# Optimization experiments

Measured on AMD Instinct MI355X. Metric: run time of the kernel, lower is better.

The kernel has to match this reference:

```python
import jax, jax.numpy as jnp
import numpy as np

HIDDEN_DIM = 1024
NUM_HEADS = 16
HEAD_DIM = HIDDEN_DIM // NUM_HEADS
SCALAR_NORM = float(np.sqrt(HIDDEN_DIM / NUM_HEADS))


def setup_inputs() -> dict:
    key = jax.random.key(0)
    k1, k2 = jax.random.split(key)
    B, N, D = 2, 2048, HIDDEN_DIM
    x = jax.random.normal(k1, (B, N, D), dtype=jnp.float32)
    # torch Linear weight shape: (3D, D); xavier_uniform-like scale
    limit = float(np.sqrt(6.0 / (D + 3 * D)))
    W_qkv = jax.random.uniform(k2, (3 * D, D), dtype=jnp.float32, minval=-limit, maxval=limit)
    return {"x": x, "W_qkv": W_qkv}


def reference(x, W_qkv):
    b, n, d = x.shape
    h, hd = NUM_HEADS, HEAD_DIM
    qkv = x @ W_qkv.T  # (B, N, 3D)
    q, k, v = jnp.split(qkv, 3, axis=-1)
    # (B, H, N, hd)
    q = q.reshape(b, n, h, hd).transpose(0, 2, 1, 3)
    k = k.reshape(b, n, h, hd).transpose(0, 2, 1, 3)
    v = v.reshape(b, n, h, hd).transpose(0, 2, 1, 3)
    scores = jnp.einsum('bhik,bhjk->bhij', q, k) / SCALAR_NORM
    attn = jax.nn.softmax(scores, axis=-1)
    out = jnp.einsum('bhij,bhjk->bhik', attn, v)
    return out.transpose(0, 2, 1, 3).reshape(b, n, d)
```

## Files before the change

### kernel.cpp

```cpp
#include <hip/hip_runtime.h>
#include <hip/hip_bf16.h>

#define SEQ 2048
#define DMODEL 1024
#define NHEADS 16
#define HD 64
#define BATCH 2

typedef short bf16x8 __attribute__((ext_vector_type(8)));
typedef float f32x4 __attribute__((ext_vector_type(4)));

static __device__ inline ushort f2bf(float f) {
    unsigned u = __float_as_uint(f);
    return (ushort)((u + 0x7fffu + ((u >> 16) & 1u)) >> 16);
}

static __device__ inline unsigned pk2bf(float a, float b) {
    __hip_bfloat162 h = __float22bfloat162_rn(make_float2(a, b));
    union { __hip_bfloat162 h; unsigned u; } c; c.h = h;
    return c.u;
}

static __device__ inline void async16(const ushort* g, ushort* l) {
    __builtin_amdgcn_global_load_lds((const __attribute__((address_space(1))) void*)g,
                                     (__attribute__((address_space(3))) void*)l, 16, 0, 0);
}

__global__ void cvt2(const float* __restrict__ a, ushort* __restrict__ da, int na,
                     const float* __restrict__ b, ushort* __restrict__ db, int nb) {
    long i = (long)(blockIdx.x * blockDim.x + threadIdx.x) * 4;
    const float* s; ushort* d;
    if (i < na) { s = a + i; d = da + i; }
    else { long j = i - na; if (j >= nb) return; s = b + j; d = db + j; }
    float4 v = *(const float4*)s;
    ushort4 o; o.x = f2bf(v.x); o.y = f2bf(v.y); o.z = f2bf(v.z); o.w = f2bf(v.w);
    *(ushort4*)d = o;
}

union GemmSmem {
    struct { ushort A[128 * 64]; ushort B[128 * 64]; } st;
    ushort C[128 * 128];
};

__global__ __launch_bounds__(256) void qkv_gemm(
        const ushort* __restrict__ X, const ushort* __restrict__ W,
        ushort* __restrict__ Qd, ushort* __restrict__ Kd, ushort* __restrict__ Vd) {
    __shared__ GemmSmem sm;
    const int t = threadIdx.x;
    const int lane = t & 63, l15 = lane & 15, quad = lane >> 4;
    const int w = t >> 6, wm = w >> 1, wn = w & 1;
    const int gm = blockIdx.x, gn = blockIdx.y;
    const int srow = t >> 3, scol = (t & 7) * 8;

    f32x4 acc[4][4] = {};

    for (int kt = 0; kt < 16; ++kt) {
        const int k0 = kt * 64;
        __syncthreads();
#pragma unroll
        for (int inst = 0; inst < 4; ++inst) {
            async16(&X[(gm * 128 + inst * 32 + srow) * 1024 + k0 + scol], &sm.st.A[inst * 2048 + t * 8]);
            async16(&W[(gn * 128 + inst * 32 + srow) * 1024 + k0 + scol], &sm.st.B[inst * 2048 + t * 8]);
        }
        __syncthreads();
#pragma unroll
        for (int ks = 0; ks < 2; ++ks) {
            const int kk = ks * 32 + quad * 8;
            bf16x8 af[4], bfr[4];
#pragma unroll
            for (int i = 0; i < 4; ++i) {
                af[i]  = *(const bf16x8*)&sm.st.A[(wm * 64 + i * 16 + l15) * 64 + kk];
                bfr[i] = *(const bf16x8*)&sm.st.B[(wn * 64 + i * 16 + l15) * 64 + kk];
            }
#pragma unroll
            for (int i = 0; i < 4; ++i)
#pragma unroll
                for (int j = 0; j < 4; ++j)
                    acc[i][j] = __builtin_amdgcn_mfma_f32_16x16x32_bf16(af[i], bfr[j], acc[i][j], 0, 0, 0);
        }
    }

    __syncthreads();
    const float sc = (gn < 8) ? (0.125f * 1.44269504f) : 1.0f;
#pragma unroll
    for (int i = 0; i < 4; ++i)
#pragma unroll
        for (int reg = 0; reg < 4; ++reg) {
            const int row = wm * 64 + i * 16 + quad * 4 + reg;
            const int sw = (row & 7) * 8;
#pragma unroll
            for (int jp = 0; jp < 4; jp += 2) {
                unsigned u = pk2bf(acc[i][jp][reg] * sc, acc[i][jp + 1][reg] * sc);
                sm.C[row * 128 + ((wn * 64 + jp * 16 + l15) ^ sw)] = (ushort)u;
                sm.C[row * 128 + ((wn * 64 + (jp + 1) * 16 + l15) ^ sw)] = (ushort)(u >> 16);
            }
        }
    __syncthreads();

    const int which = gn >> 3;
    ushort* dst = (which == 0) ? Qd : ((which == 1) ? Kd : Vd);
    const int rloc = t >> 4, l = t & 15;
#pragma unroll
    for (int pass = 0; pass < 8; ++pass) {
        const int r = pass * 16 + rloc;
        bf16x8 v = *(const bf16x8*)&sm.C[r * 128 + ((l * 8) ^ ((r & 7) * 8))];
        const int ng = gm * 128 + r;
        const int b = ng >> 11, n = ng & 2047;
        const int cl = (gn * 128 + l * 8) & 1023;
        const int h = cl >> 6, hd = cl & 63;
        *(bf16x8*)&dst[(((b * NHEADS + h) * SEQ) + n) * HD + hd] = v;
    }
}

__global__ __launch_bounds__(256) void tr_v(const ushort* __restrict__ src, ushort* __restrict__ dst) {
    __shared__ ushort sT[64][72];
    const int t = threadIdx.x;
    const int bh = blockIdx.y, nt = blockIdx.x;
    const int r0 = t >> 3, c8 = (t & 7) * 8;
    const ushort* sp = src + ((long)bh * SEQ + nt * 64) * HD;
#pragma unroll
    for (int rr = 0; rr < 64; rr += 32)
        *(bf16x8*)&sT[rr + r0][c8] = *(const bf16x8*)&sp[(rr + r0) * HD + c8];
    __syncthreads();
    ushort* dp = dst + (long)bh * HD * SEQ + nt * 64;
#pragma unroll
    for (int rr = 0; rr < 64; rr += 32) {
        const int hd = rr + r0;
        bf16x8 v;
#pragma unroll
        for (int j = 0; j < 8; ++j) v[j] = (short)sT[c8 + j][hd];
        *(bf16x8*)&dp[(long)hd * SEQ + c8] = v;
    }
}

__global__ __launch_bounds__(128, 2) void attn_kernel(
        const ushort* __restrict__ Q, const ushort* __restrict__ K,
        const ushort* __restrict__ VT, float* __restrict__ O) {
    __shared__ ushort sK[64][72];
    __shared__ ushort sVT[64][72];
    __shared__ ushort sP[64][72];
    const int t = threadIdx.x;
    const int lane = t & 63, l15 = lane & 15, quad = lane >> 4;
    const int w = t >> 6;
    const int qt = blockIdx.x, bh = blockIdx.y;
    const ushort* Qp = Q + ((long)bh * SEQ + qt * 64) * HD;
    const ushort* Kp = K + (long)bh * SEQ * HD;
    const ushort* Vp = VT + (long)bh * HD * SEQ;
    const int r0 = t >> 3, c8 = (t & 7) * 8;

    bf16x8 aq[2][2];
#pragma unroll
    for (int st = 0; st < 2; ++st)
#pragma unroll
        for (int kc = 0; kc < 2; ++kc)
            aq[st][kc] = *(const bf16x8*)&Qp[(w * 32 + st * 16 + l15) * HD + kc * 32 + quad * 8];

    f32x4 accO[2][4] = {};
    f32x4 accL[2] = {};
    bf16x8 ones;
#pragma unroll
    for (int j = 0; j < 8; ++j) ones[j] = (short)0x3F80;

    for (int kt = 0; kt < 32; ++kt) {
        __syncthreads();
#pragma unroll
        for (int rr = 0; rr < 64; rr += 16) {
            *(bf16x8*)&sK[rr + r0][c8]  = *(const bf16x8*)&Kp[(kt * 64 + rr + r0) * HD + c8];
            *(bf16x8*)&sVT[rr + r0][c8] = *(const bf16x8*)&Vp[(rr + r0) * SEQ + kt * 64 + c8];
        }
        __syncthreads();

        f32x4 s[2][4];
#pragma unroll
        for (int st = 0; st < 2; ++st)
#pragma unroll
            for (int nb = 0; nb < 4; ++nb) {
                f32x4 z = {};
                z = __builtin_amdgcn_mfma_f32_16x16x32_bf16(aq[st][0], *(const bf16x8*)&sK[nb * 16 + l15][quad * 8], z, 0, 0, 0);
                z = __builtin_amdgcn_mfma_f32_16x16x32_bf16(aq[st][1], *(const bf16x8*)&sK[nb * 16 + l15][32 + quad * 8], z, 0, 0, 0);
                s[st][nb] = z;
            }

#pragma unroll
        for (int st = 0; st < 2; ++st)
#pragma unroll
            for (int r = 0; r < 4; ++r) {
                const int row = w * 32 + st * 16 + quad * 4 + r;
#pragma unroll
                for (int nb = 0; nb < 4; nb += 2) {
                    unsigned u = pk2bf(exp2f(s[st][nb][r]), exp2f(s[st][nb + 1][r]));
                    sP[row][(nb * 16 + l15) ^ (quad << 4)] = (ushort)u;
                    sP[row][((nb + 1) * 16 + l15) ^ (quad << 4)] = (ushort)(u >> 16);
                }
            }

        bf16x8 ap[2][2];
#pragma unroll
        for (int st = 0; st < 2; ++st)
#pragma unroll
            for (int kb = 0; kb < 2; ++kb)
                ap[st][kb] = *(const bf16x8*)&sP[w * 32 + st * 16 + l15][(kb * 32 + quad * 8) ^ ((l15 & 12) << 2)];

#pragma unroll
        for (int st = 0; st < 2; ++st) {
#pragma unroll
            for (int ob = 0; ob < 4; ++ob)
#pragma unroll
                for (int kb = 0; kb < 2; ++kb)
                    accO[st][ob] = __builtin_amdgcn_mfma_f32_16x16x32_bf16(
                        ap[st][kb], *(const bf16x8*)&sVT[ob * 16 + l15][kb * 32 + quad * 8], accO[st][ob], 0, 0, 0);
#pragma unroll
            for (int kb = 0; kb < 2; ++kb)
                accL[st] = __builtin_amdgcn_mfma_f32_16x16x32_bf16(ap[st][kb], ones, accL[st], 0, 0, 0);
        }
    }

    const int b = bh >> 4, h = bh & 15;
#pragma unroll
    for (int st = 0; st < 2; ++st)
#pragma unroll
        for (int r = 0; r < 4; ++r) {
            const float inv = 1.0f / accL[st][r];
            const int row = qt * 64 + w * 32 + st * 16 + quad * 4 + r;
#pragma unroll
            for (int ob = 0; ob < 4; ++ob)
                O[((long)b * SEQ + row) * DMODEL + h * HD + ob * 16 + l15] = accO[st][ob][r] * inv;
        }
}

extern "C" void kernel_launch(void* const* d_in, const int* in_sizes, int n_in,
                              void* d_out, int out_size, void* d_ws, size_t ws_size,
                              hipStream_t stream) {
    const float* x  = (const float*)d_in[0];
    const float* Wq = (const float*)d_in[1];
    float* out = (float*)d_out;

    const int NX = BATCH * SEQ * DMODEL;
    const int NW = 3 * DMODEL * DMODEL;
    const int NQKV = BATCH * NHEADS * SEQ * HD;

    ushort* xb = (ushort*)d_ws;
    ushort* wb = xb + NX;
    ushort* q  = wb + NW;
    ushort* k  = q + NQKV;
    ushort* vtmp = k + NQKV;
    ushort* vt = xb;

    cvt2<<<(NX + NW) / 4 / 256, 256, 0, stream>>>(x, xb, NX, Wq, wb, NW);

    dim3 g1(4096 / 128, 3072 / 128);
    qkv_gemm<<<g1, 256, 0, stream>>>(xb, wb, q, k, vtmp);

    dim3 gt(SEQ / 64, BATCH * NHEADS);
    tr_v<<<gt, 256, 0, stream>>>(vtmp, vt);

    dim3 g2(SEQ / 64, BATCH * NHEADS);
    attn_kernel<<<g2, 128, 0, stream>>>(q, k, vt, out);
}
```

Before: 194.6 us.

## Restructure attention kernel with 32x32 MFMA, register softmax, double-buffered async K/V

The attention kernel now runs 8 waves per block over 256 query rows and uses 32x32x16 MFMA with S computed transposed, so P stays in registers and is repacked via v_permlane32_swap instead of going through shared memory. K and V^T tiles are double-buffered with global_load_lds async copies into XOR-swizzled LDS, and the row sum is kept as a register accumulator instead of an extra MFMA against ones. A remapped block index groups heads for locality, and setprio hints favour MFMA issue. The goal is more K/V reuse per block, fewer LDS round trips and barriers, and overlap of loads with compute, at the cost of higher register pressure and reliance on the permlane/swizzle layout being correct.

```diff
diff --git a/kernel.cpp b/kernel.cpp
--- a/kernel.cpp
+++ b/kernel.cpp
@@ -9,6 +9,7 @@
 
 typedef short bf16x8 __attribute__((ext_vector_type(8)));
 typedef float f32x4 __attribute__((ext_vector_type(4)));
+typedef float f32x16 __attribute__((ext_vector_type(16)));
 
 static __device__ inline ushort f2bf(float f) {
     unsigned u = __float_as_uint(f);
@@ -24,6 +25,10 @@
 static __device__ inline void async16(const ushort* g, ushort* l) {
     __builtin_amdgcn_global_load_lds((const __attribute__((address_space(1))) void*)g,
                                      (__attribute__((address_space(3))) void*)l, 16, 0, 0);
+}
+
+static __device__ inline void plane32swap(unsigned& a, unsigned& b) {
+    asm volatile("v_permlane32_swap_b32 %0, %1" : "+v"(a), "+v"(b));
 }
 
 __global__ void cvt2(const float* __restrict__ a, ushort* __restrict__ da, int na,
@@ -133,99 +138,119 @@
     }
 }
 
-__global__ __launch_bounds__(128, 2) void attn_kernel(
+__global__ __launch_bounds__(512, 2) void attn_kernel(
         const ushort* __restrict__ Q, const ushort* __restrict__ K,
         const ushort* __restrict__ VT, float* __restrict__ O) {
-    __shared__ ushort sK[64][72];
-    __shared__ ushort sVT[64][72];
-    __shared__ ushort sP[64][72];
+    __shared__ ushort sK[2][64 * 64];
+    __shared__ ushort sVT[2][64 * 64];
+    __shared__ float sL[8][32];
+
     const int t = threadIdx.x;
-    const int lane = t & 63, l15 = lane & 15, quad = lane >> 4;
+    const int lane = t & 63, l31 = lane & 31, hi = lane >> 5;
     const int w = t >> 6;
-    const int qt = blockIdx.x, bh = blockIdx.y;
-    const ushort* Qp = Q + ((long)bh * SEQ + qt * 64) * HD;
+
+    const int flat = blockIdx.y * gridDim.x + blockIdx.x;
+    const int qt = (flat >> 3) & 7;
+    const int bh = (flat & 7) + ((flat >> 6) << 3);
+
+    const ushort* Qp = Q + ((long)bh * SEQ + qt * 256 + w * 32) * HD;
     const ushort* Kp = K + (long)bh * SEQ * HD;
     const ushort* Vp = VT + (long)bh * HD * SEQ;
-    const int r0 = t >> 3, c8 = (t & 7) * 8;
-
-    bf16x8 aq[2][2];
-#pragma unroll
-    for (int st = 0; st < 2; ++st)
-#pragma unroll
-        for (int kc = 0; kc < 2; ++kc)
-            aq[st][kc] = *(const bf16x8*)&Qp[(w * 32 + st * 16 + l15) * HD + kc * 32 + quad * 8];
-
-    f32x4 accO[2][4] = {};
-    f32x4 accL[2] = {};
-    bf16x8 ones;
-#pragma unroll
-    for (int j = 0; j < 8; ++j) ones[j] = (short)0x3F80;
+
+    bf16x8 bq[4];
+#pragma unroll
+    for (int ks = 0; ks < 4; ++ks)
+        bq[ks] = *(const bf16x8*)&Qp[l31 * HD + ks * 16 + hi * 8];
+
+    const int sr = t >> 3;
+    const int scc = ((t & 7) ^ (sr & 7)) * 8;
+    const ushort* gK = Kp + sr * HD + scc;
+    const ushort* gV = Vp + (long)sr * SEQ + scc;
+    ushort* lK[2] = { &sK[0][t * 8], &sK[1][t * 8] };
+    ushort* lV[2] = { &sVT[0][t * 8], &sVT[1][t * 8] };
+
+    f32x16 accO[2] = {};
+    float Lp = 0.f;
+    const int swz = (l31 & 7) << 3;
+
+    async16(gK, lK[0]);
+    async16(gV, lV[0]);
+    __syncthreads();
 
     for (int kt = 0; kt < 32; ++kt) {
+        const int cur = kt & 1;
+        if (kt < 31) {
+            async16(gK + (kt + 1) * 64 * HD, lK[cur ^ 1]);
+            async16(gV + (kt + 1) * 64,      lV[cur ^ 1]);
+        }
+        const ushort* bK = sK[cur];
+        const ushort* bV = sVT[cur];
+
+        f32x16 s[2];
+#pragma unroll
+        for (int nb = 0; nb < 2; ++nb) {
+            f32x16 z = {};
+            __builtin_amdgcn_s_setprio(1);
+#pragma unroll
+            for (int ks = 0; ks < 4; ++ks) {
+                bf16x8 ak = *(const bf16x8*)&bK[(nb * 32 + l31) * 64 + ((ks * 16 + hi * 8) ^ swz)];
+                z = __builtin_amdgcn_mfma_f32_32x32x16_bf16(ak, bq[ks], z, 0, 0, 0);
+            }
+            __builtin_amdgcn_s_setprio(0);
+            s[nb] = z;
+        }
+
+        bf16x8 pa[4];
+#pragma unroll
+        for (int nb = 0; nb < 2; ++nb) {
+            float p[16];
+#pragma unroll
+            for (int r = 0; r < 16; ++r) { p[r] = exp2f(s[nb][r]); Lp += p[r]; }
+#pragma unroll
+            for (int h2 = 0; h2 < 2; ++h2) {
+                const int b = 8 * h2;
+                unsigned c0 = pk2bf(p[b + 0], p[b + 1]);
+                unsigned c1 = pk2bf(p[b + 2], p[b + 3]);
+                unsigned c2 = pk2bf(p[b + 4], p[b + 5]);
+                unsigned c3 = pk2bf(p[b + 6], p[b + 7]);
+                plane32swap(c0, c2);
+                plane32swap(c1, c3);
+                union { unsigned u[4]; bf16x8 v; } f;
+                f.u[0] = c0; f.u[1] = c1; f.u[2] = c2; f.u[3] = c3;
+                pa[nb * 2 + h2] = f.v;
+            }
+        }
+
+        __builtin_amdgcn_s_setprio(1);
+#pragma unroll
+        for (int db = 0; db < 2; ++db)
+#pragma unroll
+            for (int ks = 0; ks < 4; ++ks) {
+                bf16x8 vf = *(const bf16x8*)&bV[(db * 32 + l31) * 64 + ((ks * 16 + hi * 8) ^ swz)];
+                accO[db] = __builtin_amdgcn_mfma_f32_32x32x16_bf16(pa[ks], vf, accO[db], 0, 0, 0);
+            }
+        __builtin_amdgcn_s_setprio(0);
+
         __syncthreads();
-#pragma unroll
-        for (int rr = 0; rr < 64; rr += 16) {
-            *(bf16x8*)&sK[rr + r0][c8]  = *(const bf16x8*)&Kp[(kt * 64 + rr + r0) * HD + c8];
-            *(bf16x8*)&sVT[rr + r0][c8] = *(const bf16x8*)&Vp[(rr + r0) * SEQ + kt * 64 + c8];
-        }
-        __syncthreads();
-
-        f32x4 s[2][4];
-#pragma unroll
-        for (int st = 0; st < 2; ++st)
-#pragma unroll
-            for (int nb = 0; nb < 4; ++nb) {
-                f32x4 z = {};
-                z = __builtin_amdgcn_mfma_f32_16x16x32_bf16(aq[st][0], *(const bf16x8*)&sK[nb * 16 + l15][quad * 8], z, 0, 0, 0);
-                z = __builtin_amdgcn_mfma_f32_16x16x32_bf16(aq[st][1], *(const bf16x8*)&sK[nb * 16 + l15][32 + quad * 8], z, 0, 0, 0);
-                s[st][nb] = z;
-            }
-
-#pragma unroll
-        for (int st = 0; st < 2; ++st)
-#pragma unroll
-            for (int r = 0; r < 4; ++r) {
-                const int row = w * 32 + st * 16 + quad * 4 + r;
-#pragma unroll
-                for (int nb = 0; nb < 4; nb += 2) {
-                    unsigned u = pk2bf(exp2f(s[st][nb][r]), exp2f(s[st][nb + 1][r]));
-                    sP[row][(nb * 16 + l15) ^ (quad << 4)] = (ushort)u;
-                    sP[row][((nb + 1) * 16 + l15) ^ (quad << 4)] = (ushort)(u >> 16);
-                }
-            }
-
-        bf16x8 ap[2][2];
-#pragma unroll
-        for (int st = 0; st < 2; ++st)
-#pragma unroll
-            for (int kb = 0; kb < 2; ++kb)
-                ap[st][kb] = *(const bf16x8*)&sP[w * 32 + st * 16 + l15][(kb * 32 + quad * 8) ^ ((l15 & 12) << 2)];
-
-#pragma unroll
-        for (int st = 0; st < 2; ++st) {
-#pragma unroll
-            for (int ob = 0; ob < 4; ++ob)
-#pragma unroll
-                for (int kb = 0; kb < 2; ++kb)
-                    accO[st][ob] = __builtin_amdgcn_mfma_f32_16x16x32_bf16(
-                        ap[st][kb], *(const bf16x8*)&sVT[ob * 16 + l15][kb * 32 + quad * 8], accO[st][ob], 0, 0, 0);
-#pragma unroll
-            for (int kb = 0; kb < 2; ++kb)
-                accL[st] = __builtin_amdgcn_mfma_f32_16x16x32_bf16(ap[st][kb], ones, accL[st], 0, 0, 0);
-        }
-    }
+    }
+
+    unsigned lu = __float_as_uint(Lp), lv = lu;
+    plane32swap(lu, lv);
+    const float Ltot = __uint_as_float(lu) + __uint_as_float(lv);
+    if (hi == 0) sL[w][l31] = Ltot;
+    __syncthreads();
 
     const int b = bh >> 4, h = bh & 15;
-#pragma unroll
-    for (int st = 0; st < 2; ++st)
-#pragma unroll
-        for (int r = 0; r < 4; ++r) {
-            const float inv = 1.0f / accL[st][r];
-            const int row = qt * 64 + w * 32 + st * 16 + quad * 4 + r;
-#pragma unroll
-            for (int ob = 0; ob < 4; ++ob)
-                O[((long)b * SEQ + row) * DMODEL + h * HD + ob * 16 + l15] = accO[st][ob][r] * inv;
-        }
+    const int qg0 = qt * 256 + w * 32;
+#pragma unroll
+    for (int r = 0; r < 16; ++r) {
+        const int ql = (r & 3) + 8 * (r >> 2) + 4 * hi;
+        const float inv = 1.0f / sL[w][ql];
+        const int row = qg0 + ql;
+#pragma unroll
+        for (int db = 0; db < 2; ++db)
+            O[((long)b * SEQ + row) * DMODEL + h * HD + db * 32 + l31] = accO[db][r] * inv;
+    }
 }
 
 extern "C" void kernel_launch(void* const* d_in, const int* in_sizes, int n_in,
@@ -254,6 +279,6 @@
     dim3 gt(SEQ / 64, BATCH * NHEADS);
     tr_v<<<gt, 256, 0, stream>>>(vtmp, vt);
 
-    dim3 g2(SEQ / 64, BATCH * NHEADS);
-    attn_kernel<<<g2, 128, 0, stream>>>(q, k, vt, out);
-}
+    dim3 g2(SEQ / 256, BATCH * NHEADS);
+    attn_kernel<<<g2, 512, 0, stream>>>(q, k, vt, out);
+}
```

Measured after the change: 179.0 us. -8.0%, faster.
